# Performance work log

Measured on AMD Instinct MI355X. Metric: run time of the kernel, lower is better.

The kernel has to match this reference:

```python
import jax, jax.numpy as jnp
import numpy as np

N, DIM, K = 65536, 512, 256


def setup_inputs() -> dict:
    key = jax.random.key(0)
    k1, k2 = jax.random.split(key)
    embeddings = jax.random.normal(k1, (N, DIM), dtype=jnp.float32)
    # Centroid table produced by the (external, non-differentiable) faiss
    # k-means fit; materialized here as a learned parameter.
    centroids = jax.random.normal(k2, (K, DIM), dtype=jnp.float32)
    return {"embeddings": embeddings, "centroids": centroids, "batch_id": 0}


def reference(embeddings, centroids, batch_id):
    # Batched equivalent of the Python loop over samples:
    # for each embedding, cdist to centroids, take the 2nd-nearest centroid.
    # Squared L2 preserves the ordering of torch.cdist (monotone sqrt),
    # and the output is a gather of centroids, so math is identical.
    # d2: [N, K]
    d2 = (
        jnp.sum(embeddings * embeddings, axis=1, keepdims=True)
        - 2.0 * jnp.einsum("nd,kd->nk", embeddings, centroids)
        + jnp.sum(centroids * centroids, axis=1)
    )
    # top-2 smallest distances -> indices of nearest and 2nd-nearest centroids
    _, top2_idx = jax.lax.top_k(-d2, 2)  # [N, 2]
    hard_neg_idx = top2_idx[:, 1]  # second-nearest centroid per sample
    return centroids[hard_neg_idx]  # [N, DIM]
```

## Files before the change

### kernel.cpp

```cpp
#include <hip/hip_runtime.h>

#define N_EMB 65536
#define DIM   512
#define K_C   256
#define NCHUNK (DIM / 32)


typedef __attribute__((ext_vector_type(4))) float        f32x4;
typedef __attribute__((ext_vector_type(8))) __bf16       bf16x8;
typedef __attribute__((ext_vector_type(8))) short        s16x8;
typedef __attribute__((ext_vector_type(4))) unsigned int u32x4;

template <class T>
__device__ inline auto mfma_bf16_t(T a, T b, f32x4 c, int)
    -> decltype(__builtin_amdgcn_mfma_f32_16x16x32_bf16(a, b, c, 0, 0, 0)) {
  return __builtin_amdgcn_mfma_f32_16x16x32_bf16(a, b, c, 0, 0, 0);
}
template <class T>
__device__ inline f32x4 mfma_bf16_t(T a, T b, f32x4 c, long) {
  return __builtin_amdgcn_mfma_f32_16x16x32_bf16(
      __builtin_bit_cast(s16x8, a), __builtin_bit_cast(s16x8, b), c, 0, 0, 0);
}
__device__ inline f32x4 MFMA(bf16x8 a, bf16x8 b, f32x4 c) {
  return mfma_bf16_t(a, b, c, 0);
}

__device__ inline unsigned umin_(unsigned a, unsigned b) { return a < b ? a : b; }
__device__ inline unsigned umax_(unsigned a, unsigned b) { return a > b ? a : b; }

__device__ inline void split8(const float4 a, const float4 b, u32x4& hw, u32x4& lw) {
  const float v[8] = {a.x, a.y, a.z, a.w, b.x, b.y, b.z, b.w};
  unsigned hp[4], lp[4];
#pragma unroll
  for (int i = 0; i < 4; ++i) {
    const unsigned u0 = __float_as_uint(v[2 * i]);
    const unsigned u1 = __float_as_uint(v[2 * i + 1]);
    hp[i] = (u0 >> 16) | (u1 & 0xFFFF0000u);
    const float r0 = v[2 * i]     - __uint_as_float(u0 & 0xFFFF0000u);
    const float r1 = v[2 * i + 1] - __uint_as_float(u1 & 0xFFFF0000u);
    lp[i] = (__float_as_uint(r0) >> 16) | (__float_as_uint(r1) & 0xFFFF0000u);
  }
  hw = (u32x4){hp[0], hp[1], hp[2], hp[3]};
  lw = (u32x4){lp[0], lp[1], lp[2], lp[3]};
}

__device__ inline u32x4 cvt8hi(const float4 a, const float4 b) {
  float v[8] = {a.x, a.y, a.z, a.w, b.x, b.y, b.z, b.w};
  unsigned h[8];
#pragma unroll
  for (int i = 0; i < 8; ++i) {
    const unsigned u = __float_as_uint(v[i]);
    h[i] = (u + 0x7FFFu + ((u >> 16) & 1u)) >> 16;
  }
  return (u32x4){h[0] | (h[1] << 16), h[2] | (h[3] << 16),
                 h[4] | (h[5] << 16), h[6] | (h[7] << 16)};
}

__global__ void pack_centroids(const float* __restrict__ cent,
                               unsigned* __restrict__ cbh,
                               float* __restrict__ cnorm) {
  const int k    = blockIdx.x;
  const int lane = threadIdx.x;
  const float* src = cent + (size_t)k * DIM + lane * 8;
  const float4 a = *(const float4*)src;
  const float4 b = *(const float4*)(src + 4);
  const int chunk = lane >> 2, g = lane & 3;
  ((u32x4*)cbh)[((size_t)chunk * 16 + (k >> 4)) * 64 + g * 16 + (k & 15)] =
      cvt8hi(a, b);
  float s = a.x * a.x + a.y * a.y + a.z * a.z + a.w * a.w +
            b.x * b.x + b.y * b.y + b.z * b.z + b.w * b.w;
#pragma unroll
  for (int off = 32; off > 0; off >>= 1) s += __shfl_down(s, off, 64);
  if (lane == 0) cnorm[k] = s;
}

__global__ __launch_bounds__(256, 2)
void neg_sampler_main(const float* __restrict__ emb,
                      const float* __restrict__ cent,
                      const unsigned* __restrict__ cbh,
                      const float* __restrict__ cnorm,
                      float* __restrict__ out) {
  __shared__ unsigned top4s[4][32][4];

  const int tid  = threadIdx.x;
  const int lane = tid & 63;
  const int w    = tid >> 6;
  const int row0 = (blockIdx.x * 4 + w) * 32;
  const int frow = lane & 15, fgrp = lane >> 4;

  f32x4 acc[2][16];
#pragma unroll
  for (int i = 0; i < 2; ++i)
#pragma unroll
    for (int j = 0; j < 16; ++j) acc[i][j] = (f32x4){0.f, 0.f, 0.f, 0.f};

  const float* const e0p = emb + (size_t)(row0 + frow) * DIM + fgrp * 8;
  const float* const e1p = e0p + (size_t)16 * DIM;

  float4 a0 = *(const float4*)(e0p);
  float4 b0 = *(const float4*)(e0p + 4);
  float4 a1 = *(const float4*)(e1p);
  float4 b1 = *(const float4*)(e1p + 4);

  for (int c = 0; c < NCHUNK; ++c) {
    const int cn = (c + 1) & (NCHUNK - 1);
    const float4 na0 = *(const float4*)(e0p + cn * 32);
    const float4 nb0 = *(const float4*)(e0p + cn * 32 + 4);
    const float4 na1 = *(const float4*)(e1p + cn * 32);
    const float4 nb1 = *(const float4*)(e1p + cn * 32 + 4);

    const u32x4* cs = (const u32x4*)cbh + (size_t)c * 1024 + lane;
    u32x4 cc[16];
#pragma unroll
    for (int ct = 0; ct < 16; ++ct) cc[ct] = cs[ct * 64];

    u32x4 h0, l0, h1, l1;
    split8(a0, b0, h0, l0);
    split8(a1, b1, h1, l1);
    const bf16x8 eh0 = __builtin_bit_cast(bf16x8, h0);
    const bf16x8 el0 = __builtin_bit_cast(bf16x8, l0);
    const bf16x8 eh1 = __builtin_bit_cast(bf16x8, h1);
    const bf16x8 el1 = __builtin_bit_cast(bf16x8, l1);

#pragma unroll
    for (int ct = 0; ct < 16; ++ct) {
      const bf16x8 ch = __builtin_bit_cast(bf16x8, cc[ct]);
      acc[0][ct] = MFMA(eh0, ch, acc[0][ct]);
      acc[1][ct] = MFMA(eh1, ch, acc[1][ct]);
      acc[0][ct] = MFMA(el0, ch, acc[0][ct]);
      acc[1][ct] = MFMA(el1, ch, acc[1][ct]);
    }
    a0 = na0; b0 = nb0; a1 = na1; b1 = nb1;
  }

  const int lcol = lane & 15, lgrp = lane >> 4;
  float cnv[16];
#pragma unroll
  for (int ct = 0; ct < 16; ++ct) cnv[ct] = cnorm[ct * 16 + lcol];

#pragma unroll
  for (int rt = 0; rt < 2; ++rt) {
#pragma unroll
    for (int rg = 0; rg < 4; ++rg) {
      unsigned b0_ = 0xFFFFFFFFu, b1_ = b0_, b2_ = b0_, b3_ = b0_;
      auto ins = [&](unsigned u) {
        b3_ = umin_(b3_, umax_(b2_, u));
        b2_ = umin_(b2_, umax_(b1_, u));
        b1_ = umin_(b1_, umax_(b0_, u));
        b0_ = umin_(b0_, u);
      };
#pragma unroll
      for (int ct = 0; ct < 16; ++ct) {
        const float s = fmaf(-2.f, acc[rt][ct][rg], cnv[ct]);
        ins((__float_as_uint(s) & 0xFFFFFF00u) | (unsigned)(ct * 16 + lcol));
      }
#pragma unroll
      for (int off = 1; off < 16; off <<= 1) {
        const unsigned o0 = __shfl_xor(b0_, off, 64);
        const unsigned o1 = __shfl_xor(b1_, off, 64);
        const unsigned o2 = __shfl_xor(b2_, off, 64);
        const unsigned o3 = __shfl_xor(b3_, off, 64);
        ins(o0); ins(o1); ins(o2); ins(o3);
      }
      if (lcol == 0) {
        const int rl = rt * 16 + lgrp * 4 + rg;
        *(u32x4*)&top4s[w][rl][0] = (u32x4){b0_, b1_, b2_, b3_};
      }
    }
  }

  for (int rr = 0; rr < 32; ++rr) {
    const int grow = row0 + rr;
    const int c0 = (int)(top4s[w][rr][0] & 0xFFu);
    const int c1 = (int)(top4s[w][rr][1] & 0xFFu);
    const int c2 = (int)(top4s[w][rr][2] & 0xFFu);
    const int c3 = (int)(top4s[w][rr][3] & 0xFFu);

    const float4* e4 = (const float4*)(emb + (size_t)grow * DIM) + lane * 2;
    const float4 ev0 = e4[0], ev1 = e4[1];

    auto pdot = [&](int cj) {
      const float4* c4 = (const float4*)(cent + (size_t)cj * DIM) + lane * 2;
      const float4 cv0 = c4[0], cv1 = c4[1];
      float d = ev0.x * cv0.x;
      d = fmaf(ev0.y, cv0.y, d); d = fmaf(ev0.z, cv0.z, d); d = fmaf(ev0.w, cv0.w, d);
      d = fmaf(ev1.x, cv1.x, d); d = fmaf(ev1.y, cv1.y, d);
      d = fmaf(ev1.z, cv1.z, d); d = fmaf(ev1.w, cv1.w, d);
      return d;
    };
    float d0 = pdot(c0), d1 = pdot(c1), d2 = pdot(c2), d3 = pdot(c3);
#pragma unroll
    for (int off = 1; off < 64; off <<= 1) {
      d0 += __shfl_xor(d0, off, 64);
      d1 += __shfl_xor(d1, off, 64);
      d2 += __shfl_xor(d2, off, 64);
      d3 += __shfl_xor(d3, off, 64);
    }
    const float s0 = fmaf(-2.f, d0, cnorm[c0]);
    const float s1 = fmaf(-2.f, d1, cnorm[c1]);
    const float s2 = fmaf(-2.f, d2, cnorm[c2]);
    const float s3 = fmaf(-2.f, d3, cnorm[c3]);

    float v1 = s0, v2 = 3.4e38f;
    int i1 = c0, i2 = K_C;
    auto upd = [&](float s, int ci) {
      if (s < v1 || (s == v1 && ci < i1)) { v2 = v1; i2 = i1; v1 = s; i1 = ci; }
      else if (s < v2 || (s == v2 && ci < i2)) { v2 = s; i2 = ci; }
    };
    upd(s1, c1); upd(s2, c2); upd(s3, c3);

    const float4* sp = (const float4*)(cent + (size_t)i2 * DIM) + lane * 2;
    float4* op = (float4*)(out + (size_t)grow * DIM) + lane * 2;
    op[0] = sp[0];
    op[1] = sp[1];
  }
}

extern "C" void kernel_launch(void* const* d_in, const int* in_sizes, int n_in,
                              void* d_out, int out_size, void* d_ws, size_t ws_size,
                              hipStream_t stream) {
  (void)in_sizes; (void)n_in; (void)out_size; (void)ws_size;
  const float* emb  = (const float*)d_in[0];
  const float* cent = (const float*)d_in[1];
  unsigned* cbh = (unsigned*)d_ws;
  float* cnorm  = (float*)((char*)d_ws + 256 * 1024);

  pack_centroids<<<K_C, 64, 0, stream>>>(cent, cbh, cnorm);
  neg_sampler_main<<<N_EMB / 128, 256, 0, stream>>>(emb, cent, cbh, cnorm,
                                                    (float*)d_out);
}
```

Measured before the change: 325.5 us.

## Drop low-order bf16 correction pass and halve rows per wave

The embedding is now truncated to a single bf16 term instead of a hi+lo split, which halves MFMA work in the coarse top-4 screening pass. Rows per wave drop from 32 to 16, launch bounds rise to 4 blocks per CU, and centroid fragments are loaded in two groups of eight to cut register pressure and raise occupancy. Final selection still uses an exact fp32 rescoring of the top-4 candidates, but the coarser screen makes it more likely that the true second-nearest centroid falls outside the top 4.

```diff
diff --git a/kernel.cpp b/kernel.cpp
--- a/kernel.cpp
+++ b/kernel.cpp
@@ -4,6 +4,8 @@
 #define DIM   512
 #define K_C   256
 #define NCHUNK (DIM / 32)
+#define RPW   16
+#define WAVES 4
 
 
 typedef __attribute__((ext_vector_type(4))) float        f32x4;
@@ -28,23 +30,15 @@
 __device__ inline unsigned umin_(unsigned a, unsigned b) { return a < b ? a : b; }
 __device__ inline unsigned umax_(unsigned a, unsigned b) { return a > b ? a : b; }
 
-__device__ inline void split8(const float4 a, const float4 b, u32x4& hw, u32x4& lw) {
-  const float v[8] = {a.x, a.y, a.z, a.w, b.x, b.y, b.z, b.w};
-  unsigned hp[4], lp[4];
-#pragma unroll
-  for (int i = 0; i < 4; ++i) {
-    const unsigned u0 = __float_as_uint(v[2 * i]);
-    const unsigned u1 = __float_as_uint(v[2 * i + 1]);
-    hp[i] = (u0 >> 16) | (u1 & 0xFFFF0000u);
-    const float r0 = v[2 * i]     - __uint_as_float(u0 & 0xFFFF0000u);
-    const float r1 = v[2 * i + 1] - __uint_as_float(u1 & 0xFFFF0000u);
-    lp[i] = (__float_as_uint(r0) >> 16) | (__float_as_uint(r1) & 0xFFFF0000u);
-  }
-  hw = (u32x4){hp[0], hp[1], hp[2], hp[3]};
-  lw = (u32x4){lp[0], lp[1], lp[2], lp[3]};
-}
-
-__device__ inline u32x4 cvt8hi(const float4 a, const float4 b) {
+__device__ inline u32x4 pack8hi(const float4 a, const float4 b) {
+  return (u32x4){
+      (__float_as_uint(a.x) >> 16) | (__float_as_uint(a.y) & 0xFFFF0000u),
+      (__float_as_uint(a.z) >> 16) | (__float_as_uint(a.w) & 0xFFFF0000u),
+      (__float_as_uint(b.x) >> 16) | (__float_as_uint(b.y) & 0xFFFF0000u),
+      (__float_as_uint(b.z) >> 16) | (__float_as_uint(b.w) & 0xFFFF0000u)};
+}
+
+__device__ inline u32x4 cvt8hi_rne(const float4 a, const float4 b) {
   float v[8] = {a.x, a.y, a.z, a.w, b.x, b.y, b.z, b.w};
   unsigned h[8];
 #pragma unroll
@@ -66,7 +60,7 @@
   const float4 b = *(const float4*)(src + 4);
   const int chunk = lane >> 2, g = lane & 3;
   ((u32x4*)cbh)[((size_t)chunk * 16 + (k >> 4)) * 64 + g * 16 + (k & 15)] =
-      cvt8hi(a, b);
+      cvt8hi_rne(a, b);
   float s = a.x * a.x + a.y * a.y + a.z * a.z + a.w * a.w +
             b.x * b.x + b.y * b.y + b.z * b.z + b.w * b.w;
 #pragma unroll
@@ -74,63 +68,50 @@
   if (lane == 0) cnorm[k] = s;
 }
 
-__global__ __launch_bounds__(256, 2)
+__global__ __launch_bounds__(256, 4)
 void neg_sampler_main(const float* __restrict__ emb,
                       const float* __restrict__ cent,
                       const unsigned* __restrict__ cbh,
                       const float* __restrict__ cnorm,
                       float* __restrict__ out) {
-  __shared__ unsigned top4s[4][32][4];
+  __shared__ unsigned top4s[WAVES][RPW][4];
 
   const int tid  = threadIdx.x;
   const int lane = tid & 63;
   const int w    = tid >> 6;
-  const int row0 = (blockIdx.x * 4 + w) * 32;
+  const int row0 = (blockIdx.x * WAVES + w) * RPW;
   const int frow = lane & 15, fgrp = lane >> 4;
 
-  f32x4 acc[2][16];
-#pragma unroll
-  for (int i = 0; i < 2; ++i)
-#pragma unroll
-    for (int j = 0; j < 16; ++j) acc[i][j] = (f32x4){0.f, 0.f, 0.f, 0.f};
-
-  const float* const e0p = emb + (size_t)(row0 + frow) * DIM + fgrp * 8;
-  const float* const e1p = e0p + (size_t)16 * DIM;
-
-  float4 a0 = *(const float4*)(e0p);
-  float4 b0 = *(const float4*)(e0p + 4);
-  float4 a1 = *(const float4*)(e1p);
-  float4 b1 = *(const float4*)(e1p + 4);
+  f32x4 acc[16];
+#pragma unroll
+  for (int j = 0; j < 16; ++j) acc[j] = (f32x4){0.f, 0.f, 0.f, 0.f};
+
+  const float* const ep = emb + (size_t)(row0 + frow) * DIM + fgrp * 8;
+
+  float4 a0 = *(const float4*)(ep);
+  float4 b0 = *(const float4*)(ep + 4);
 
   for (int c = 0; c < NCHUNK; ++c) {
     const int cn = (c + 1) & (NCHUNK - 1);
-    const float4 na0 = *(const float4*)(e0p + cn * 32);
-    const float4 nb0 = *(const float4*)(e0p + cn * 32 + 4);
-    const float4 na1 = *(const float4*)(e1p + cn * 32);
-    const float4 nb1 = *(const float4*)(e1p + cn * 32 + 4);
+    const float4 na = *(const float4*)(ep + cn * 32);
+    const float4 nb = *(const float4*)(ep + cn * 32 + 4);
+
+    const bf16x8 eh = __builtin_bit_cast(bf16x8, pack8hi(a0, b0));
 
     const u32x4* cs = (const u32x4*)cbh + (size_t)c * 1024 + lane;
-    u32x4 cc[16];
-#pragma unroll
-    for (int ct = 0; ct < 16; ++ct) cc[ct] = cs[ct * 64];
-
-    u32x4 h0, l0, h1, l1;
-    split8(a0, b0, h0, l0);
-    split8(a1, b1, h1, l1);
-    const bf16x8 eh0 = __builtin_bit_cast(bf16x8, h0);
-    const bf16x8 el0 = __builtin_bit_cast(bf16x8, l0);
-    const bf16x8 eh1 = __builtin_bit_cast(bf16x8, h1);
-    const bf16x8 el1 = __builtin_bit_cast(bf16x8, l1);
-
-#pragma unroll
-    for (int ct = 0; ct < 16; ++ct) {
-      const bf16x8 ch = __builtin_bit_cast(bf16x8, cc[ct]);
-      acc[0][ct] = MFMA(eh0, ch, acc[0][ct]);
-      acc[1][ct] = MFMA(eh1, ch, acc[1][ct]);
-      acc[0][ct] = MFMA(el0, ch, acc[0][ct]);
-      acc[1][ct] = MFMA(el1, ch, acc[1][ct]);
-    }
-    a0 = na0; b0 = nb0; a1 = na1; b1 = nb1;
+    u32x4 cc[8];
+#pragma unroll
+    for (int ct = 0; ct < 8; ++ct) cc[ct] = cs[ct * 64];
+#pragma unroll
+    for (int ct = 0; ct < 8; ++ct)
+      acc[ct] = MFMA(eh, __builtin_bit_cast(bf16x8, cc[ct]), acc[ct]);
+#pragma unroll
+    for (int ct = 0; ct < 8; ++ct) cc[ct] = cs[(ct + 8) * 64];
+#pragma unroll
+    for (int ct = 0; ct < 8; ++ct)
+      acc[ct + 8] = MFMA(eh, __builtin_bit_cast(bf16x8, cc[ct]), acc[ct + 8]);
+
+    a0 = na; b0 = nb;
   }
 
   const int lcol = lane & 15, lgrp = lane >> 4;
@@ -139,37 +120,34 @@
   for (int ct = 0; ct < 16; ++ct) cnv[ct] = cnorm[ct * 16 + lcol];
 
 #pragma unroll
-  for (int rt = 0; rt < 2; ++rt) {
-#pragma unroll
-    for (int rg = 0; rg < 4; ++rg) {
-      unsigned b0_ = 0xFFFFFFFFu, b1_ = b0_, b2_ = b0_, b3_ = b0_;
-      auto ins = [&](unsigned u) {
-        b3_ = umin_(b3_, umax_(b2_, u));
-        b2_ = umin_(b2_, umax_(b1_, u));
-        b1_ = umin_(b1_, umax_(b0_, u));
-        b0_ = umin_(b0_, u);
-      };
-#pragma unroll
-      for (int ct = 0; ct < 16; ++ct) {
-        const float s = fmaf(-2.f, acc[rt][ct][rg], cnv[ct]);
-        ins((__float_as_uint(s) & 0xFFFFFF00u) | (unsigned)(ct * 16 + lcol));
-      }
-#pragma unroll
-      for (int off = 1; off < 16; off <<= 1) {
-        const unsigned o0 = __shfl_xor(b0_, off, 64);
-        const unsigned o1 = __shfl_xor(b1_, off, 64);
-        const unsigned o2 = __shfl_xor(b2_, off, 64);
-        const unsigned o3 = __shfl_xor(b3_, off, 64);
-        ins(o0); ins(o1); ins(o2); ins(o3);
-      }
-      if (lcol == 0) {
-        const int rl = rt * 16 + lgrp * 4 + rg;
-        *(u32x4*)&top4s[w][rl][0] = (u32x4){b0_, b1_, b2_, b3_};
-      }
-    }
-  }
-
-  for (int rr = 0; rr < 32; ++rr) {
+  for (int rg = 0; rg < 4; ++rg) {
+    unsigned b0_ = 0xFFFFFFFFu, b1_ = b0_, b2_ = b0_, b3_ = b0_;
+    auto ins = [&](unsigned u) {
+      b3_ = umin_(b3_, umax_(b2_, u));
+      b2_ = umin_(b2_, umax_(b1_, u));
+      b1_ = umin_(b1_, umax_(b0_, u));
+      b0_ = umin_(b0_, u);
+    };
+#pragma unroll
+    for (int ct = 0; ct < 16; ++ct) {
+      const float s = fmaf(-2.f, acc[ct][rg], cnv[ct]);
+      ins((__float_as_uint(s) & 0xFFFFFF00u) | (unsigned)(ct * 16 + lcol));
+    }
+#pragma unroll
+    for (int off = 1; off < 16; off <<= 1) {
+      const unsigned o0 = __shfl_xor(b0_, off, 64);
+      const unsigned o1 = __shfl_xor(b1_, off, 64);
+      const unsigned o2 = __shfl_xor(b2_, off, 64);
+      const unsigned o3 = __shfl_xor(b3_, off, 64);
+      ins(o0); ins(o1); ins(o2); ins(o3);
+    }
+    if (lcol == 0) {
+      const int rl = lgrp * 4 + rg;
+      *(u32x4*)&top4s[w][rl][0] = (u32x4){b0_, b1_, b2_, b3_};
+    }
+  }
+
+  for (int rr = 0; rr < RPW; ++rr) {
     const int grow = row0 + rr;
     const int c0 = (int)(top4s[w][rr][0] & 0xFFu);
     const int c1 = (int)(top4s[w][rr][1] & 0xFFu);
@@ -226,6 +204,6 @@
   float* cnorm  = (float*)((char*)d_ws + 256 * 1024);
 
   pack_centroids<<<K_C, 64, 0, stream>>>(cent, cbh, cnorm);
-  neg_sampler_main<<<N_EMB / 128, 256, 0, stream>>>(emb, cent, cbh, cnorm,
-                                                    (float*)d_out);
-}
+  neg_sampler_main<<<N_EMB / (WAVES * RPW), 256, 0, stream>>>(emb, cent, cbh,
+                                                              cnorm, (float*)d_out);
+}
```

Result: no change. 321.0 us (-1.4%).
